# Performance work log

Hardware: AMD Instinct MI355X
Metric: run time of the kernel (lower is better)

## Reference

```python
import jax, jax.numpy as jnp
import numpy as np

K = 7            # neighborhood kernel size
HEADS = 4
DIMS = [64, 64, 64, 64]
POOL = 2
MLP_NAT = 4      # mlp_ratio for NAT layers
MLP_GA = 3       # mlp_ratio for GlobalAttention


def _ln(x, g, b, eps=1e-5):
    m = x.mean(-1, keepdims=True)
    v = ((x - m) ** 2).mean(-1, keepdims=True)
    return (x - m) * jax.lax.rsqrt(v + eps) * g + b


def _nbr(L, k):
    # NATTEN-style clamped window: start in [0, L-k]
    i = jnp.arange(L)
    start = jnp.clip(i - k // 2, 0, L - k)
    idx = start[:, None] + jnp.arange(k)          # [L,k] neighbor coords
    rel = idx - i[:, None] + (k - 1)              # [L,k] rpb index in [0,2k-2]
    return idx, rel


def _nat_attn(x, qkv_w, qkv_b, rpb, proj_w, proj_b):
    B, H, W, C = x.shape
    d = C // HEADS
    qkv = (x @ qkv_w + qkv_b).reshape(B, H, W, 3, HEADS, d)
    q = qkv[..., 0, :, :].transpose(0, 3, 1, 2, 4) * (d ** -0.5)  # [B,h,H,W,d]
    kk = qkv[..., 1, :, :].transpose(0, 3, 1, 2, 4)
    vv = qkv[..., 2, :, :].transpose(0, 3, 1, 2, 4)
    iy, ry = _nbr(H, K)
    ix, rx = _nbr(W, K)
    k_nb = kk[:, :, iy][:, :, :, :, ix]   # [B,h,H,K,W,K,d]
    v_nb = vv[:, :, iy][:, :, :, :, ix]
    attn = jnp.einsum('bhijd,bhiajcd->bhijac', q, k_nb)  # [B,h,H,W,K,K]
    bias = rpb[:, ry][:, :, :, rx]                        # [h,H,K,W,K]
    attn = attn + bias.transpose(0, 1, 3, 2, 4)[None]
    B_, h_, H_, W_ = attn.shape[:4]
    attn = jax.nn.softmax(attn.reshape(B_, h_, H_, W_, K * K), axis=-1)
    attn = attn.reshape(B_, h_, H_, W_, K, K)
    out = jnp.einsum('bhijac,bhiajcd->bhijd', attn, v_nb)
    out = out.transpose(0, 2, 3, 1, 4).reshape(B, H, W, C)
    return out @ proj_w + proj_b


def _nat_block(x, ln1g, ln1b, qw, qb, rpb, pw, pb, ln2g, ln2b, f1w, f1b, f2w, f2b):
    x = x + _nat_attn(_ln(x, ln1g, ln1b), qw, qb, rpb, pw, pb)
    h = _ln(x, ln2g, ln2b)
    h = jax.nn.gelu(h @ f1w + f1b, approximate=False) @ f2w + f2b
    return x + h


def _global_block(x, ln1g, ln1b, qw, qb, ln2g, ln2b, f1w, f1b, f2w, f2b):
    B, H, W, C = x.shape
    d = C // HEADS
    xn = _ln(x, ln1g, ln1b)
    Hp, Wp = H // POOL, W // POOL
    xa = xn.reshape(B, Hp, POOL, Wp, POOL, C).mean((2, 4)).reshape(B, Hp * Wp, C)
    N = Hp * Wp
    qkv = (xa @ qw + qb).reshape(B, N, 3, HEADS, d).transpose(2, 0, 3, 1, 4)
    q, k, v = qkv[0] * (d ** -0.5), qkv[1], qkv[2]
    attn = jax.nn.softmax(jnp.einsum('bhnd,bhmd->bhnm', q, k), axis=-1)
    o = jnp.einsum('bhnm,bhmd->bhnd', attn, v)            # [B,h,N,d]
    o = o.transpose(0, 1, 3, 2).reshape(B, C, Hp, Wp)      # (attn@v).transpose(2,3).reshape(B,C,N)
    o = jnp.repeat(jnp.repeat(o, POOL, axis=2), POOL, axis=3)  # nearest upsample
    x = x + o.transpose(0, 2, 3, 1)
    h = _ln(x, ln2g, ln2b)
    h = jax.nn.gelu(h @ f1w + f1b, approximate=False) @ f2w + f2b
    return x + h


def setup_inputs() -> dict:
    key = jax.random.key(0)
    ks = iter(jax.random.split(key, 32))
    B, H, W = 4, 56, 56
    C = DIMS[0]
    n = len(DIMS) - 1  # 3 NAT branches
    s = 0.02
    inp = {
        'x': jax.random.normal(next(ks), (B, H, W, sum(DIMS)), jnp.float32),
        'nat_ln1_g': jnp.ones((n, C)), 'nat_ln1_b': jnp.zeros((n, C)),
        'nat_qkv_w': jax.random.normal(next(ks), (n, C, 3 * C)) * s,
        'nat_qkv_b': jnp.zeros((n, 3 * C)),
        'nat_rpb': jax.random.normal(next(ks), (n, HEADS, 2 * K - 1, 2 * K - 1)) * s,
        'nat_proj_w': jax.random.normal(next(ks), (n, C, C)) * s,
        'nat_proj_b': jnp.zeros((n, C)),
        'nat_ln2_g': jnp.ones((n, C)), 'nat_ln2_b': jnp.zeros((n, C)),
        'nat_fc1_w': jax.random.normal(next(ks), (n, C, MLP_NAT * C)) * s,
        'nat_fc1_b': jnp.zeros((n, MLP_NAT * C)),
        'nat_fc2_w': jax.random.normal(next(ks), (n, MLP_NAT * C, C)) * s,
        'nat_fc2_b': jnp.zeros((n, C)),
        'ga_ln1_g': jnp.ones((C,)), 'ga_ln1_b': jnp.zeros((C,)),
        'ga_qkv_w': jax.random.normal(next(ks), (C, 3 * C)) * s,
        'ga_qkv_b': jnp.zeros((3 * C,)),
        'ga_ln2_g': jnp.ones((C,)), 'ga_ln2_b': jnp.zeros((C,)),
        'ga_fc1_w': jax.random.normal(next(ks), (C, MLP_GA * C)) * s,
        'ga_fc1_b': jnp.zeros((MLP_GA * C,)),
        'ga_fc2_w': jax.random.normal(next(ks), (MLP_GA * C, C)) * s,
        'ga_fc2_b': jnp.zeros((C,)),
    }
    return inp


def reference(x, nat_ln1_g, nat_ln1_b, nat_qkv_w, nat_qkv_b, nat_rpb, nat_proj_w,
              nat_proj_b, nat_ln2_g, nat_ln2_b, nat_fc1_w, nat_fc1_b, nat_fc2_w,
              nat_fc2_b, ga_ln1_g, ga_ln1_b, ga_qkv_w, ga_qkv_b, ga_ln2_g,
              ga_ln2_b, ga_fc1_w, ga_fc1_b, ga_fc2_w, ga_fc2_b):
    parts = jnp.split(x, np.cumsum(DIMS)[:-1].tolist(), axis=-1)
    outs = []
    for i in range(len(DIMS) - 1):
        outs.append(_nat_block(parts[i], nat_ln1_g[i], nat_ln1_b[i], nat_qkv_w[i],
                               nat_qkv_b[i], nat_rpb[i], nat_proj_w[i], nat_proj_b[i],
                               nat_ln2_g[i], nat_ln2_b[i], nat_fc1_w[i], nat_fc1_b[i],
                               nat_fc2_w[i], nat_fc2_b[i]))
    outs.append(_global_block(parts[-1], ga_ln1_g, ga_ln1_b, ga_qkv_w, ga_qkv_b,
                              ga_ln2_g, ga_ln2_b, ga_fc1_w, ga_fc1_b, ga_fc2_w, ga_fc2_b))
    return jnp.concatenate(outs, axis=-1)
```

## Files before the change

kernel.cpp:

```cpp
#include <hip/hip_runtime.h>
#include <hip/hip_bf16.h>
#include <cstdint>

namespace {

constexpr int NPIX = 12544;

typedef __attribute__((ext_vector_type(8))) short bf16x8;
typedef __attribute__((ext_vector_type(4))) float f32x4;
typedef __attribute__((ext_vector_type(16))) float f32x16;
typedef _Float16 h2 __attribute__((ext_vector_type(2)));

__device__ __forceinline__ float wsum(float v) {
#pragma unroll
  for (int m = 32; m; m >>= 1) v += __shfl_xor(v, m, 64);
  return v;
}

__device__ __forceinline__ uint16_t f2bf(float f) {
  uint32_t u = __builtin_bit_cast(uint32_t, f);
  u += 0x7fffu + ((u >> 16) & 1u);
  return (uint16_t)(u >> 16);
}
__device__ __forceinline__ uint32_t packbf(float a, float b) {
  return (uint32_t)f2bf(a) | ((uint32_t)f2bf(b) << 16);
}
__device__ __forceinline__ ushort f2h(float f) {
  _Float16 h = (_Float16)f;
  return __builtin_bit_cast(ushort, h);
}
__device__ __forceinline__ h2 bch2(uint32_t u) { return __builtin_bit_cast(h2, u); }

__device__ __forceinline__ float gelu_fast(float v) {
  float u = 0.7978845608028654f * (v + 0.044715f * v * v * v);
  float e = __expf(2.f * u);
  float th = 1.f - 2.f * __builtin_amdgcn_rcpf(e + 1.f);
  return 0.5f * v * (1.f + th);
}

__global__ __launch_bounds__(256) void k_prep(
    const float* __restrict__ nqkv, const float* __restrict__ nproj,
    const float* __restrict__ nf1, const float* __restrict__ nf2,
    const float* __restrict__ gqkv, const float* __restrict__ gf1,
    const float* __restrict__ gf2, ushort* __restrict__ wT) {
  int t = blockIdx.x * 256 + threadIdx.x;
  if (t >= 201728) return;
  int i = t;
  if (i < 41472) {
    int br = i / 13824, r = i % 13824, n = r / 72, k = r % 72;
    wT[t] = k < 64 ? f2bf(nqkv[(br * 64 + k) * 192 + n]) : (ushort)0;
    return;
  }
  i -= 41472;
  if (i < 13824) {
    int br = i / 4608, r = i % 4608, n = r / 72, k = r % 72;
    wT[t] = k < 64 ? f2bf(nproj[(br * 64 + k) * 64 + n]) : (ushort)0;
    return;
  }
  i -= 13824;
  if (i < 55296) {
    int br = i / 18432, r = i % 18432, n = r / 72, k = r % 72;
    wT[t] = k < 64 ? f2bf(nf1[(br * 64 + k) * 256 + n]) : (ushort)0;
    return;
  }
  i -= 55296;
  if (i < 50688) {
    int br = i / 16896, r = i % 16896, n = r / 264, k = r % 264;
    wT[t] = k < 256 ? f2bf(nf2[(br * 256 + k) * 64 + n]) : (ushort)0;
    return;
  }
  i -= 50688;
  if (i < 13824) {
    int n = i / 72, k = i % 72;
    wT[t] = k < 64 ? f2bf(gqkv[k * 192 + n]) : (ushort)0;
    return;
  }
  i -= 13824;
  if (i < 13824) {
    int n = i / 72, k = i % 72;
    wT[t] = k < 64 ? f2bf(gf1[k * 192 + n]) : (ushort)0;
    return;
  }
  i -= 13824;
  {
    int n = i / 200, k = i % 200;
    wT[t] = k < 192 ? f2bf(gf2[k * 64 + n]) : (ushort)0;
  }
}

__global__ __launch_bounds__(256) void k_qkv(
    const float* __restrict__ x, const float* __restrict__ nat_ln1_g,
    const float* __restrict__ nat_ln1_b, const ushort* __restrict__ wT,
    const float* __restrict__ nat_qkv_b, ushort* __restrict__ qn,
    ushort* __restrict__ kvn, const float* __restrict__ ga_ln1_g,
    const float* __restrict__ ga_ln1_b, const float* __restrict__ ga_qkv_b,
    ushort* __restrict__ qb, ushort* __restrict__ kb, ushort* __restrict__ vT) {
  __shared__ __align__(16) ushort sA[64 * 72];
  int bid = blockIdx.x;
  int tid = threadIdx.x, lane = tid & 63, wid = tid >> 6;
  if (bid == 637) {
    for (int i = tid; i < 4096; i += 256) {
      int bh = i >> 8, rem = i & 255;
      int n = 784 + (rem >> 4), d = rem & 15;
      qb[((size_t)bh * 800 + n) * 16 + d] = 0;
      kb[((size_t)bh * 800 + n) * 16 + d] = 0;
      vT[((size_t)bh * 16 + d) * 800 + n] = 0;
    }
    return;
  }
  int lr = lane & 15, lk = (lane >> 4) * 8;
  if (bid < 588) {
    int br = bid / 196, grp = bid % 196;
    const ushort* Wg = wT + br * 13824;
    float g = nat_ln1_g[br * 64 + lane], bb = nat_ln1_b[br * 64 + lane];
#pragma unroll
    for (int i = 0; i < 16; ++i) {
      int pl = wid * 16 + i;
      float v = x[(size_t)(grp * 64 + pl) * 256 + br * 64 + lane];
      float s1 = wsum(v), s2 = wsum(v * v);
      float m = s1 * (1.f / 64.f);
      float var = s2 * (1.f / 64.f) - m * m;
      sA[pl * 72 + lane] = f2bf((v - m) * rsqrtf(var + 1e-5f) * g + bb);
    }
    __syncthreads();
    int m0 = wid * 16;
    bf16x8 a0 = *(const bf16x8*)&sA[(m0 + lr) * 72 + lk];
    bf16x8 a1 = *(const bf16x8*)&sA[(m0 + lr) * 72 + 32 + lk];
    int r0 = m0 + (lane >> 4) * 4;
#pragma unroll
    for (int nt = 0; nt < 12; ++nt) {
      int n0 = nt * 16;
      bf16x8 b0 = *(const bf16x8*)&Wg[(n0 + lr) * 72 + lk];
      bf16x8 b1 = *(const bf16x8*)&Wg[(n0 + lr) * 72 + 32 + lk];
      f32x4 acc = {0.f, 0.f, 0.f, 0.f};
      acc = __builtin_amdgcn_mfma_f32_16x16x32_bf16(a0, b0, acc, 0, 0, 0);
      acc = __builtin_amdgcn_mfma_f32_16x16x32_bf16(a1, b1, acc, 0, 0, 0);
      int col = n0 + lr;
      float bias = nat_qkv_b[br * 192 + col];
      if (nt < 4) {
        ushort* op = qn + ((size_t)br * NPIX + grp * 64 + r0) * 64 + col;
#pragma unroll
        for (int r = 0; r < 4; ++r) op[r * 64] = f2h((acc[r] + bias) * 0.25f);
      } else {
        ushort* op = kvn + ((size_t)br * NPIX + grp * 64 + r0) * 128 + (col - 64);
#pragma unroll
        for (int r = 0; r < 4; ++r) op[r * 128] = f2h(acc[r] + bias);
      }
    }
  } else {
    int g64 = bid - 588;
    const ushort* Wg = wT + 161280;
    float gg = ga_ln1_g[lane], bb = ga_ln1_b[lane];
#pragma unroll
    for (int i = 0; i < 16; ++i) {
      int tl = wid * 16 + i;
      int token = g64 * 64 + tl;
      int b = token / 784, rem2 = token % 784, hp = rem2 / 28, wp = rem2 % 28;
      float s = 0.f;
#pragma unroll
      for (int dy = 0; dy < 2; ++dy)
#pragma unroll
        for (int dxx = 0; dxx < 2; ++dxx) {
          int pix = b * 3136 + (hp * 2 + dy) * 56 + (wp * 2 + dxx);
          float v = x[(size_t)pix * 256 + 192 + lane];
          float s1 = wsum(v), s2 = wsum(v * v);
          float m = s1 * (1.f / 64.f);
          float var = s2 * (1.f / 64.f) - m * m;
          s += (v - m) * rsqrtf(var + 1e-5f) * gg + bb;
        }
      sA[tl * 72 + lane] = f2bf(0.25f * s);
    }
    __syncthreads();
    int m0 = wid * 16;
    bf16x8 a0 = *(const bf16x8*)&sA[(m0 + lr) * 72 + lk];
    bf16x8 a1 = *(const bf16x8*)&sA[(m0 + lr) * 72 + 32 + lk];
    int r0 = m0 + (lane >> 4) * 4;
#pragma unroll
    for (int nt = 0; nt < 12; ++nt) {
      int n0 = nt * 16;
      bf16x8 b0 = *(const bf16x8*)&Wg[(n0 + lr) * 72 + lk];
      bf16x8 b1 = *(const bf16x8*)&Wg[(n0 + lr) * 72 + 32 + lk];
      f32x4 acc = {0.f, 0.f, 0.f, 0.f};
      acc = __builtin_amdgcn_mfma_f32_16x16x32_bf16(a0, b0, acc, 0, 0, 0);
      acc = __builtin_amdgcn_mfma_f32_16x16x32_bf16(a1, b1, acc, 0, 0, 0);
      int col = n0 + lr;
      float bias = ga_qkv_b[col];
      int hh = (col & 63) >> 4, d = col & 15;
#pragma unroll
      for (int r = 0; r < 4; ++r) {
        int token = g64 * 64 + r0 + r;
        int b = token / 784, nn = token % 784;
        float v = acc[r] + bias;
        if (col < 64)
          qb[((size_t)(b * 4 + hh) * 800 + nn) * 16 + d] = f2bf(v * 0.25f);
        else if (col < 128)
          kb[((size_t)(b * 4 + hh) * 800 + nn) * 16 + d] = f2bf(v);
        else
          vT[((size_t)(b * 4 + hh) * 16 + d) * 800 + nn] = f2bf(v);
      }
    }
  }
}

__global__ __launch_bounds__(256) void k_attn(
    const ushort* __restrict__ qn, const ushort* __restrict__ kvn,
    const float* __restrict__ rpb, const ushort* __restrict__ wT,
    const float* __restrict__ pb, const float* __restrict__ x,
    float* __restrict__ x1, const ushort* __restrict__ qb,
    const ushort* __restrict__ kb, const ushort* __restrict__ vT,
    float* __restrict__ x1g) {
  __shared__ __align__(16) ushort sBuf[196 * 72];
  int bid = blockIdx.x;
  int tid = threadIdx.x, lane = tid & 63, wid = tid >> 6;
  if (bid < 588) {
    ushort* sK = sBuf;
    int br = bid / 196, rem = bid % 196;
    int b = rem / 49, t = rem % 49;
    int y0 = (t / 7) * 8, x0 = (t % 7) * 8;
    int hy = min(max(y0 - 3, 0), 42), hx = min(max(x0 - 3, 0), 42);
    const ushort* kvbase = kvn + ((size_t)br * NPIX + b * 3136) * 128;
    for (int i = tid; i < 1568; i += 256) {
      int p = i >> 3, c = i & 7;
      int py = p / 14, px = p % 14;
      int gp = (hy + py) * 56 + (hx + px);
      *(uint4*)&sK[p * 72 + c * 8] =
          *(const uint4*)&kvbase[(size_t)gp * 128 + c * 8];
    }
    __syncthreads();
    int pl = tid & 63, h = tid >> 6;
    int ly = pl >> 3, lx = pl & 7;
    int y = y0 + ly, xg = x0 + lx;
    int sy = min(max(y - 3, 0), 49), sx = min(max(xg - 3, 0), 49);
    int by = sy - hy, bx = sx - hx;
    int gpix = b * 3136 + y * 56 + xg;
    const ushort* qp = qn + ((size_t)br * NPIX + gpix) * 64 + h * 16;
    uint4 qv0 = *(const uint4*)&qp[0];
    uint4 qv1 = *(const uint4*)&qp[8];
    h2 q[8] = {bch2(qv0.x), bch2(qv0.y), bch2(qv0.z), bch2(qv0.w),
               bch2(qv1.x), bch2(qv1.y), bch2(qv1.z), bch2(qv1.w)};
    const float* rp = rpb + (br * 4 + h) * 169 + (sy - y + 6) * 13 + (sx - xg + 6);
    h2 z = {(_Float16)0.f, (_Float16)0.f};
    float s[49];
    float mx = -1e30f;
#pragma unroll
    for (int a = 0; a < 7; ++a) {
      const ushort* krow = &sK[((by + a) * 14 + bx) * 72 + h * 16];
      const float* rpa = rp + a * 13;
#pragma unroll
      for (int c = 0; c < 7; ++c) {
        const ushort* kp = krow + c * 72;
        uint4 k0 = *(const uint4*)&kp[0];
        uint4 k1 = *(const uint4*)&kp[8];
        h2 d = z;
        d = bch2(k0.x) * q[0] + d;
        d = bch2(k0.y) * q[1] + d;
        d = bch2(k0.z) * q[2] + d;
        d = bch2(k0.w) * q[3] + d;
        d = bch2(k1.x) * q[4] + d;
        d = bch2(k1.y) * q[5] + d;
        d = bch2(k1.z) * q[6] + d;
        d = bch2(k1.w) * q[7] + d;
        float sd = (float)d[0] + (float)d[1] + rpa[c];
        s[a * 7 + c] = sd;
        mx = fmaxf(mx, sd);
      }
    }
    __syncthreads();
    for (int i = tid; i < 1568; i += 256) {
      int p = i >> 3, c = i & 7;
      int py = p / 14, px = p % 14;
      int gp = (hy + py) * 56 + (hx + px);
      *(uint4*)&sK[p * 72 + c * 8] =
          *(const uint4*)&kvbase[(size_t)gp * 128 + 64 + c * 8];
    }
    __syncthreads();
    float l = 0.f;
    h2 acc[8];
#pragma unroll
    for (int i = 0; i < 8; ++i) acc[i] = z;
#pragma unroll
    for (int a = 0; a < 7; ++a) {
      const ushort* vrow = &sK[((by + a) * 14 + bx) * 72 + h * 16];
#pragma unroll
      for (int c = 0; c < 7; ++c) {
        float p = __expf(s[a * 7 + c] - mx);
        l += p;
        h2 p2 = {(_Float16)p, (_Float16)p};
        const ushort* vp = vrow + c * 72;
        uint4 v0 = *(const uint4*)&vp[0];
        uint4 v1 = *(const uint4*)&vp[8];
        acc[0] = bch2(v0.x) * p2 + acc[0];
        acc[1] = bch2(v0.y) * p2 + acc[1];
        acc[2] = bch2(v0.z) * p2 + acc[2];
        acc[3] = bch2(v0.w) * p2 + acc[3];
        acc[4] = bch2(v1.x) * p2 + acc[4];
        acc[5] = bch2(v1.y) * p2 + acc[5];
        acc[6] = bch2(v1.z) * p2 + acc[6];
        acc[7] = bch2(v1.w) * p2 + acc[7];
      }
    }
    float inv = 1.f / l;
    __syncthreads();
    ushort* sAp = sBuf;
    uint32_t* ao = (uint32_t*)&sAp[pl * 72 + h * 16];
#pragma unroll
    for (int i = 0; i < 8; ++i)
      ao[i] = packbf((float)acc[i][0] * inv, (float)acc[i][1] * inv);
    __syncthreads();
    const ushort* Wp = wT + 41472 + br * 4608;
    int lr = lane & 15, lk = (lane >> 4) * 8;
    int m0 = wid * 16;
    bf16x8 a0 = *(const bf16x8*)&sAp[(m0 + lr) * 72 + lk];
    bf16x8 a1 = *(const bf16x8*)&sAp[(m0 + lr) * 72 + 32 + lk];
    int r0 = m0 + (lane >> 4) * 4;
#pragma unroll
    for (int nt = 0; nt < 4; ++nt) {
      int n0 = nt * 16;
      bf16x8 b0 = *(const bf16x8*)&Wp[(n0 + lr) * 72 + lk];
      bf16x8 b1 = *(const bf16x8*)&Wp[(n0 + lr) * 72 + 32 + lk];
      f32x4 oacc = {0.f, 0.f, 0.f, 0.f};
      oacc = __builtin_amdgcn_mfma_f32_16x16x32_bf16(a0, b0, oacc, 0, 0, 0);
      oacc = __builtin_amdgcn_mfma_f32_16x16x32_bf16(a1, b1, oacc, 0, 0, 0);
      int col = n0 + lr;
      float bias = pb[br * 64 + col];
#pragma unroll
      for (int r = 0; r < 4; ++r) {
        int rr = r0 + r;
        int gp2 = b * 3136 + (y0 + (rr >> 3)) * 56 + (x0 + (rr & 7));
        x1[((size_t)br * NPIX + gp2) * 64 + col] =
            oacc[r] + bias + x[(size_t)gp2 * 256 + br * 64 + col];
      }
    }
  } else {
    int wt = (bid - 588) * 4 + wid;
    int bh = wt / 25, qt = wt % 25;
    int h = bh & 3, b = bh >> 2;
    int qrow = lane & 31, hi = lane >> 5;
    int dmod = lane & 15;
    const ushort* qbase = qb + (size_t)bh * 800 * 16;
    const ushort* kbase = kb + (size_t)bh * 800 * 16;
    const ushort* vbase = vT + (size_t)bh * 16 * 800 + (size_t)dmod * 800;
    bf16x8 qf = *(const bf16x8*)&qbase[(qt * 32 + qrow) * 16 + hi * 8];
    float m = -1e30f, l = 0.f;
    f32x16 acc_o;
#pragma unroll
    for (int r = 0; r < 16; ++r) acc_o[r] = 0.f;
    bf16x8 kf = *(const bf16x8*)&kbase[(0 + qrow) * 16 + hi * 8];
    bf16x8 vf0 = *(const bf16x8*)&vbase[0 + hi * 8];
    bf16x8 vf1 = *(const bf16x8*)&vbase[16 + hi * 8];
    for (int kt = 0; kt < 25; ++kt) {
      int nb = (kt < 24 ? kt + 1 : 24) * 32;
      bf16x8 nkf = *(const bf16x8*)&kbase[(nb + qrow) * 16 + hi * 8];
      bf16x8 nvf0 = *(const bf16x8*)&vbase[nb + hi * 8];
      bf16x8 nvf1 = *(const bf16x8*)&vbase[nb + 16 + hi * 8];
      f32x16 zero;
#pragma unroll
      for (int r = 0; r < 16; ++r) zero[r] = 0.f;
      f32x16 st = __builtin_amdgcn_mfma_f32_32x32x16_bf16(kf, qf, zero, 0, 0, 0);
      float s[16];
#pragma unroll
      for (int r = 0; r < 16; ++r) s[r] = st[r];
      if (kt == 24) {
#pragma unroll
        for (int r = 8; r < 16; ++r) s[r] = -1e30f;
      }
      float tm = s[0];
#pragma unroll
      for (int r = 1; r < 16; ++r) tm = fmaxf(tm, s[r]);
      tm = fmaxf(tm, __shfl_xor(tm, 32, 64));
      if (__any(tm > m + 8.f)) {
        float mn = fmaxf(m, tm);
        float sc = __expf(m - mn);
        l *= sc;
        m = mn;
#pragma unroll
        for (int r = 0; r < 16; ++r) {
          int row = (r & 3) + 4 * hi + 8 * (r >> 2);
          float scr = __shfl(sc, row, 64);
          acc_o[r] *= scr;
        }
      }
      uint32_t pk[8];
      float ps = 0.f;
#pragma unroll
      for (int i = 0; i < 8; ++i) {
        float p0 = __expf(s[2 * i] - m), p1 = __expf(s[2 * i + 1] - m);
        ps += p0 + p1;
        pk[i] = packbf(p0, p1);
      }
      l += ps;
#pragma unroll
      for (int t = 0; t < 2; ++t) {
        uint32_t c0 = pk[4 * t + 0], c1 = pk[4 * t + 1];
        uint32_t c2 = pk[4 * t + 2], c3 = pk[4 * t + 3];
        uint32_t b00 = __shfl((int)c0, qrow, 64), b02 = __shfl((int)c2, qrow, 64);
        uint32_t b10 = __shfl((int)c1, qrow, 64), b12 = __shfl((int)c3, qrow, 64);
        uint32_t b20 = __shfl((int)c0, qrow + 32, 64), b22 = __shfl((int)c2, qrow + 32, 64);
        uint32_t b30 = __shfl((int)c1, qrow + 32, 64), b32 = __shfl((int)c3, qrow + 32, 64);
        union { uint32_t u[4]; bf16x8 v; } pa;
        pa.u[0] = hi ? b02 : b00;
        pa.u[1] = hi ? b12 : b10;
        pa.u[2] = hi ? b22 : b20;
        pa.u[3] = hi ? b32 : b30;
        acc_o = __builtin_amdgcn_mfma_f32_32x32x16_bf16(pa.v, (t ? vf1 : vf0),
                                                        acc_o, 0, 0, 0);
      }
      kf = nkf; vf0 = nvf0; vf1 = nvf1;
    }
    l += __shfl_xor(l, 32, 64);
    float inv = 1.f / l;
#pragma unroll
    for (int r = 0; r < 16; ++r) {
      int row = (r & 3) + 4 * hi + 8 * (r >> 2);
      float invr = __shfl(inv, row, 64);
      int n = qt * 32 + row;
      if (n < 784 && qrow < 16) {
        float o = acc_o[r] * invr;
        int hp = n / 28, wp = n % 28;
        int ch = h * 16 + dmod;
#pragma unroll
        for (int dy = 0; dy < 2; ++dy)
#pragma unroll
          for (int dxx = 0; dxx < 2; ++dxx) {
            int pix = b * 3136 + (hp * 2 + dy) * 56 + (wp * 2 + dxx);
            x1g[(size_t)pix * 64 + ch] = x[(size_t)pix * 256 + 192 + ch] + o;
          }
      }
    }
  }
}

template <bool NAT>
__device__ __forceinline__ void mlp_body(
    int br, int grp, ushort* sX, ushort* sH,
    const float* __restrict__ x1, const ushort* __restrict__ W1,
    const ushort* __restrict__ W2, const float* __restrict__ B1,
    const float* __restrict__ B2, const float* __restrict__ G,
    const float* __restrict__ Bt, float* __restrict__ out) {
  constexpr int H1 = NAT ? 256 : 192;
  constexpr int K2P = NAT ? 264 : 200;
  constexpr int KB = H1 / 32;
  int tid = threadIdx.x, lane = tid & 63, wid = tid >> 6;
  const float* xin = x1 + ((size_t)br * NPIX + grp * 64) * 64;
  float g = G[lane], bb = Bt[lane];
#pragma unroll
  for (int i = 0; i < 16; ++i) {
    int pl = wid * 16 + i;
    float v = xin[pl * 64 + lane];
    float s1 = wsum(v), s2 = wsum(v * v);
    float m = s1 * (1.f / 64.f);
    float var = s2 * (1.f / 64.f) - m * m;
    sX[pl * 72 + lane] = f2bf((v - m) * rsqrtf(var + 1e-5f) * g + bb);
  }
  __syncthreads();
  int lr = lane & 15, lk = (lane >> 4) * 8;
  int mbase = (wid & 1) * 16;
  int r0 = (lane >> 4) * 4;
  bf16x8 a0[2], a1[2];
#pragma unroll
  for (int mh = 0; mh < 2; ++mh) {
    int m0 = mh * 32 + mbase;
    a0[mh] = *(const bf16x8*)&sX[(m0 + lr) * 72 + lk];
    a1[mh] = *(const bf16x8*)&sX[(m0 + lr) * 72 + 32 + lk];
  }
#pragma unroll
  for (int t2 = 0; t2 < H1 / 32; ++t2) {
    int n0 = ((wid >> 1) + 2 * t2) * 16;
    bf16x8 b0 = *(const bf16x8*)&W1[(n0 + lr) * 72 + lk];
    bf16x8 b1 = *(const bf16x8*)&W1[(n0 + lr) * 72 + 32 + lk];
    int col = n0 + lr;
    float b1v = B1[col];
#pragma unroll
    for (int mh = 0; mh < 2; ++mh) {
      f32x4 acc = {0.f, 0.f, 0.f, 0.f};
      acc = __builtin_amdgcn_mfma_f32_16x16x32_bf16(a0[mh], b0, acc, 0, 0, 0);
      acc = __builtin_amdgcn_mfma_f32_16x16x32_bf16(a1[mh], b1, acc, 0, 0, 0);
      int m0 = mh * 32 + mbase;
#pragma unroll
      for (int r = 0; r < 4; ++r) {
        int row = m0 + r0 + r;
        sH[row * K2P + (col ^ (((row >> 2) & 3) << 3))] =
            f2bf(gelu_fast(acc[r] + b1v));
      }
    }
  }
  __syncthreads();
#pragma unroll
  for (int mh = 0; mh < 2; ++mh) {
    int m0 = mh * 32 + mbase;
    bf16x8 af[KB];
#pragma unroll
    for (int kb = 0; kb < KB; ++kb) {
      int arow = m0 + lr;
      af[kb] = *(const bf16x8*)&sH[arow * K2P +
                                   ((kb * 32 + lk) ^ (((arow >> 2) & 3) << 3))];
    }
#pragma unroll
    for (int u = 0; u < 2; ++u) {
      int n0 = ((wid >> 1) + 2 * u) * 16;
      f32x4 acc = {0.f, 0.f, 0.f, 0.f};
#pragma unroll
      for (int kb = 0; kb < KB; ++kb) {
        bf16x8 bf = *(const bf16x8*)&W2[(n0 + lr) * K2P + kb * 32 + lk];
        acc = __builtin_amdgcn_mfma_f32_16x16x32_bf16(af[kb], bf, acc, 0, 0, 0);
      }
      int col = n0 + lr;
      float b2v = B2[col];
#pragma unroll
      for (int r = 0; r < 4; ++r) {
        int p = m0 + r0 + r;
        int pix = grp * 64 + p;
        out[(size_t)pix * 256 + br * 64 + col] = xin[p * 64 + col] + acc[r] + b2v;
      }
    }
  }
}

__global__ __launch_bounds__(256) void k_mlp(
    const float* __restrict__ x1, const float* __restrict__ nat_ln2_g,
    const float* __restrict__ nat_ln2_b, const ushort* __restrict__ wT,
    const float* __restrict__ nat_f1b, const float* __restrict__ nat_f2b,
    const float* __restrict__ ga_ln2_g, const float* __restrict__ ga_ln2_b,
    const float* __restrict__ ga_f1b, const float* __restrict__ ga_f2b,
    float* __restrict__ out) {
  __shared__ __align__(16) ushort sX[64 * 72];
  __shared__ __align__(16) ushort sH[64 * 264];
  int bid = blockIdx.x;
  if (bid < 588) {
    int br = bid / 196, grp = bid % 196;
    mlp_body<true>(br, grp, sX, sH, x1, wT + 55296 + br * 18432,
                   wT + 110592 + br * 16896, nat_f1b + br * 256,
                   nat_f2b + br * 64, nat_ln2_g + br * 64, nat_ln2_b + br * 64,
                   out);
  } else {
    int grp = bid - 588;
    mlp_body<false>(3, grp, sX, sH, x1, wT + 175104, wT + 188928, ga_f1b,
                    ga_f2b, ga_ln2_g, ga_ln2_b, out);
  }
}

}

extern "C" void kernel_launch(void* const* d_in, const int* in_sizes, int n_in,
                              void* d_out, int out_size, void* d_ws, size_t ws_size,
                              hipStream_t stream) {
  const float* x = (const float*)d_in[0];
  const float* nat_ln1_g = (const float*)d_in[1];
  const float* nat_ln1_b = (const float*)d_in[2];
  const float* nat_qkv_w = (const float*)d_in[3];
  const float* nat_qkv_b = (const float*)d_in[4];
  const float* nat_rpb = (const float*)d_in[5];
  const float* nat_proj_w = (const float*)d_in[6];
  const float* nat_proj_b = (const float*)d_in[7];
  const float* nat_ln2_g = (const float*)d_in[8];
  const float* nat_ln2_b = (const float*)d_in[9];
  const float* nat_fc1_w = (const float*)d_in[10];
  const float* nat_fc1_b = (const float*)d_in[11];
  const float* nat_fc2_w = (const float*)d_in[12];
  const float* nat_fc2_b = (const float*)d_in[13];
  const float* ga_ln1_g = (const float*)d_in[14];
  const float* ga_ln1_b = (const float*)d_in[15];
  const float* ga_qkv_w = (const float*)d_in[16];
  const float* ga_qkv_b = (const float*)d_in[17];
  const float* ga_ln2_g = (const float*)d_in[18];
  const float* ga_ln2_b = (const float*)d_in[19];
  const float* ga_fc1_w = (const float*)d_in[20];
  const float* ga_fc1_b = (const float*)d_in[21];
  const float* ga_fc2_w = (const float*)d_in[22];
  const float* ga_fc2_b = (const float*)d_in[23];

  uint8_t* w8 = (uint8_t*)d_ws;
  ushort* qn  = (ushort*)w8;
  ushort* kvn = (ushort*)(w8 + 4816896);
  float*  x1  = (float*)(w8 + 14450688);
  ushort* wT  = (ushort*)(w8 + 27295744);
  ushort* qgb = (ushort*)(w8 + 27699200);
  ushort* kgb = (ushort*)(w8 + 28108800);
  ushort* vgT = (ushort*)(w8 + 28518400);

  k_prep<<<dim3(789), dim3(256), 0, stream>>>(nat_qkv_w, nat_proj_w, nat_fc1_w,
                                              nat_fc2_w, ga_qkv_w, ga_fc1_w,
                                              ga_fc2_w, wT);
  k_qkv<<<dim3(638), dim3(256), 0, stream>>>(x, nat_ln1_g, nat_ln1_b, wT,
                                             nat_qkv_b, qn, kvn, ga_ln1_g,
                                             ga_ln1_b, ga_qkv_b, qgb, kgb, vgT);
  k_attn<<<dim3(688), dim3(256), 0, stream>>>(qn, kvn, nat_rpb, wT, nat_proj_b,
                                              x, x1, qgb, kgb, vgT,
                                              x1 + (size_t)3 * NPIX * 64);
  k_mlp<<<dim3(784), dim3(256), 0, stream>>>(x1, nat_ln2_g, nat_ln2_b, wT,
                                             nat_fc1_b, nat_fc2_b, ga_ln2_g,
                                             ga_ln2_b, ga_fc1_b, ga_fc2_b,
                                             (float*)d_out);
}
```

Before: 85.20 us.

## Remap blocks per XCD, batch global loads, prefetch V tile into registers

Block IDs in the three kernels are remapped so that consecutive logical blocks land on the same XCD, which should improve L2 locality on the multi-die GPU. The LayerNorm input loads are hoisted into register arrays so that all loads are issued before the shuffle reductions. In the attention kernel, the V halo tile is loaded into registers together with the K tile and later written to shared memory, so its global latency overlaps the QK/softmax phase. The cost is higher register pressure, which may reduce occupancy, and the remap relies on exact grid sizes (638, 688, 784).

```diff
diff --git a/kernel.cpp b/kernel.cpp
--- a/kernel.cpp
+++ b/kernel.cpp
@@ -96,7 +96,9 @@
     const float* __restrict__ ga_ln1_b, const float* __restrict__ ga_qkv_b,
     ushort* __restrict__ qb, ushort* __restrict__ kb, ushort* __restrict__ vT) {
   __shared__ __align__(16) ushort sA[64 * 72];
-  int bid = blockIdx.x;
+  int o = blockIdx.x;
+  int xcd = o & 7, idx = o >> 3;
+  int bid = (xcd < 6 ? xcd * 80 : 480 + (xcd - 6) * 79) + idx;
   int tid = threadIdx.x, lane = tid & 63, wid = tid >> 6;
   if (bid == 637) {
     for (int i = tid; i < 4096; i += 256) {
@@ -113,10 +115,14 @@
     int br = bid / 196, grp = bid % 196;
     const ushort* Wg = wT + br * 13824;
     float g = nat_ln1_g[br * 64 + lane], bb = nat_ln1_b[br * 64 + lane];
+    float xv[16];
+#pragma unroll
+    for (int i = 0; i < 16; ++i)
+      xv[i] = x[(size_t)(grp * 64 + wid * 16 + i) * 256 + br * 64 + lane];
 #pragma unroll
     for (int i = 0; i < 16; ++i) {
       int pl = wid * 16 + i;
-      float v = x[(size_t)(grp * 64 + pl) * 256 + br * 64 + lane];
+      float v = xv[i];
       float s1 = wsum(v), s2 = wsum(v * v);
       float m = s1 * (1.f / 64.f);
       float var = s2 * (1.f / 64.f) - m * m;
@@ -156,18 +162,23 @@
       int tl = wid * 16 + i;
       int token = g64 * 64 + tl;
       int b = token / 784, rem2 = token % 784, hp = rem2 / 28, wp = rem2 % 28;
-      float s = 0.f;
+      float v4[4];
 #pragma unroll
       for (int dy = 0; dy < 2; ++dy)
 #pragma unroll
         for (int dxx = 0; dxx < 2; ++dxx) {
           int pix = b * 3136 + (hp * 2 + dy) * 56 + (wp * 2 + dxx);
-          float v = x[(size_t)pix * 256 + 192 + lane];
-          float s1 = wsum(v), s2 = wsum(v * v);
-          float m = s1 * (1.f / 64.f);
-          float var = s2 * (1.f / 64.f) - m * m;
-          s += (v - m) * rsqrtf(var + 1e-5f) * gg + bb;
+          v4[dy * 2 + dxx] = x[(size_t)pix * 256 + 192 + lane];
         }
+      float s = 0.f;
+#pragma unroll
+      for (int k = 0; k < 4; ++k) {
+        float v = v4[k];
+        float s1 = wsum(v), s2 = wsum(v * v);
+        float m = s1 * (1.f / 64.f);
+        float var = s2 * (1.f / 64.f) - m * m;
+        s += (v - m) * rsqrtf(var + 1e-5f) * gg + bb;
+      }
       sA[tl * 72 + lane] = f2bf(0.25f * s);
     }
     __syncthreads();
@@ -210,7 +221,8 @@
     const ushort* __restrict__ kb, const ushort* __restrict__ vT,
     float* __restrict__ x1g) {
   __shared__ __align__(16) ushort sBuf[196 * 72];
-  int bid = blockIdx.x;
+  int o = blockIdx.x;
+  int bid = (o & 7) * 86 + (o >> 3);
   int tid = threadIdx.x, lane = tid & 63, wid = tid >> 6;
   if (bid < 588) {
     ushort* sK = sBuf;
@@ -219,14 +231,6 @@
     int y0 = (t / 7) * 8, x0 = (t % 7) * 8;
     int hy = min(max(y0 - 3, 0), 42), hx = min(max(x0 - 3, 0), 42);
     const ushort* kvbase = kvn + ((size_t)br * NPIX + b * 3136) * 128;
-    for (int i = tid; i < 1568; i += 256) {
-      int p = i >> 3, c = i & 7;
-      int py = p / 14, px = p % 14;
-      int gp = (hy + py) * 56 + (hx + px);
-      *(uint4*)&sK[p * 72 + c * 8] =
-          *(const uint4*)&kvbase[(size_t)gp * 128 + c * 8];
-    }
-    __syncthreads();
     int pl = tid & 63, h = tid >> 6;
     int ly = pl >> 3, lx = pl & 7;
     int y = y0 + ly, xg = x0 + lx;
@@ -236,6 +240,25 @@
     const ushort* qp = qn + ((size_t)br * NPIX + gpix) * 64 + h * 16;
     uint4 qv0 = *(const uint4*)&qp[0];
     uint4 qv1 = *(const uint4*)&qp[8];
+    for (int i = tid; i < 1568; i += 256) {
+      int p = i >> 3, c = i & 7;
+      int py = p / 14, px = p % 14;
+      int gp = (hy + py) * 56 + (hx + px);
+      *(uint4*)&sK[p * 72 + c * 8] =
+          *(const uint4*)&kvbase[(size_t)gp * 128 + c * 8];
+    }
+    uint4 vreg[7];
+#pragma unroll
+    for (int j = 0; j < 7; ++j) {
+      int i = j * 256 + tid;
+      if (j < 6 || tid < 32) {
+        int p = i >> 3, c = i & 7;
+        int py = p / 14, px = p % 14;
+        int gp = (hy + py) * 56 + (hx + px);
+        vreg[j] = *(const uint4*)&kvbase[(size_t)gp * 128 + 64 + c * 8];
+      }
+    }
+    __syncthreads();
     h2 q[8] = {bch2(qv0.x), bch2(qv0.y), bch2(qv0.z), bch2(qv0.w),
                bch2(qv1.x), bch2(qv1.y), bch2(qv1.z), bch2(qv1.w)};
     const float* rp = rpb + (br * 4 + h) * 169 + (sy - y + 6) * 13 + (sx - xg + 6);
@@ -266,12 +289,13 @@
       }
     }
     __syncthreads();
-    for (int i = tid; i < 1568; i += 256) {
-      int p = i >> 3, c = i & 7;
-      int py = p / 14, px = p % 14;
-      int gp = (hy + py) * 56 + (hx + px);
-      *(uint4*)&sK[p * 72 + c * 8] =
-          *(const uint4*)&kvbase[(size_t)gp * 128 + 64 + c * 8];
+#pragma unroll
+    for (int j = 0; j < 7; ++j) {
+      int i = j * 256 + tid;
+      if (j < 6 || tid < 32) {
+        int p = i >> 3, c = i & 7;
+        *(uint4*)&sK[p * 72 + c * 8] = vreg[j];
+      }
     }
     __syncthreads();
     float l = 0.f;
@@ -443,10 +467,14 @@
   int tid = threadIdx.x, lane = tid & 63, wid = tid >> 6;
   const float* xin = x1 + ((size_t)br * NPIX + grp * 64) * 64;
   float g = G[lane], bb = Bt[lane];
+  float xv[16];
+#pragma unroll
+  for (int i = 0; i < 16; ++i)
+    xv[i] = xin[(wid * 16 + i) * 64 + lane];
 #pragma unroll
   for (int i = 0; i < 16; ++i) {
     int pl = wid * 16 + i;
-    float v = xin[pl * 64 + lane];
+    float v = xv[i];
     float s1 = wsum(v), s2 = wsum(v * v);
     float m = s1 * (1.f / 64.f);
     float var = s2 * (1.f / 64.f) - m * m;
@@ -525,7 +553,8 @@
     float* __restrict__ out) {
   __shared__ __align__(16) ushort sX[64 * 72];
   __shared__ __align__(16) ushort sH[64 * 264];
-  int bid = blockIdx.x;
+  int o = blockIdx.x;
+  int bid = (o & 7) * 98 + (o >> 3);
   if (bid < 588) {
     int br = bid / 196, grp = bid % 196;
     mlp_body<true>(br, grp, sX, sH, x1, wT + 55296 + br * 18432,
```

After: 103.4 us. 1.21x slower.
